# Performance work log

Measured on AMD Instinct MI355X. Metric: run time of the kernel, lower is better.

## Reference

```python
import jax, jax.numpy as jnp
import numpy as np
import math

B, TSRC, TTGT, DM, DI, H = 2, 2048, 2048, 1024, 1024, 16
DH = DI // H
LN_EPS = 1e-5


def setup_inputs() -> dict:
    key = jax.random.key(0)
    ks = iter(jax.random.split(key, 40))
    def p(*shape):
        return jax.random.normal(next(ks), shape, jnp.float32) * 0.02
    inp = {
        "enc_out_vecs": jax.random.normal(next(ks), (B, TSRC, DM), jnp.float32),
        "output_vecs": jax.random.normal(next(ks), (B, TTGT, DM), jnp.float32),
    }
    for tag in ("dd", "ed"):
        inp["Wq_" + tag] = p(DM, DI); inp["bq_" + tag] = jnp.zeros((DI,), jnp.float32)
        inp["Wk_" + tag] = p(DM, DI); inp["bk_" + tag] = jnp.zeros((DI,), jnp.float32)
        inp["Wv_" + tag] = p(DM, DI); inp["bv_" + tag] = jnp.zeros((DI,), jnp.float32)
        inp["Wo_" + tag] = p(DI, DM); inp["bo_" + tag] = jnp.zeros((DM,), jnp.float32)
        inp["W1_" + tag] = p(DM, 2 * DM); inp["b1_" + tag] = jnp.zeros((2 * DM,), jnp.float32)
        inp["W2_" + tag] = p(2 * DM, DM); inp["b2_" + tag] = jnp.zeros((DM,), jnp.float32)
        inp["g1_" + tag] = jnp.ones((DM,), jnp.float32); inp["be1_" + tag] = jnp.zeros((DM,), jnp.float32)
        inp["g2_" + tag] = jnp.ones((DM,), jnp.float32); inp["be2_" + tag] = jnp.zeros((DM,), jnp.float32)
    return inp


def _ln(x, g, b):
    m = jnp.mean(x, axis=-1, keepdims=True)
    v = jnp.var(x, axis=-1, keepdims=True)
    return (x - m) * jax.lax.rsqrt(v + LN_EPS) * g + b


def _mha(xq, xkv, Wq, bq, Wk, bk, Wv, bv, causal):
    Bb, Tq, _ = xq.shape
    Tk = xkv.shape[1]
    q = (xq @ Wq + bq).reshape(Bb, Tq, H, DH)
    k = (xkv @ Wk + bk).reshape(Bb, Tk, H, DH)
    v = (xkv @ Wv + bv).reshape(Bb, Tk, H, DH)
    s = jnp.einsum("bqhd,bkhd->bhqk", q, k) / math.sqrt(DH)
    if causal:
        mask = jnp.where(jnp.arange(Tk)[None, :] > jnp.arange(Tq)[:, None], -jnp.inf, 0.0)
        s = s + mask
    w = jax.nn.softmax(s, axis=-1)
    return jnp.einsum("bhqk,bkhd->bqhd", w, v).reshape(Bb, Tq, H * DH)


def reference(enc_out_vecs, output_vecs,
              Wq_dd, bq_dd, Wk_dd, bk_dd, Wv_dd, bv_dd, Wo_dd, bo_dd,
              W1_dd, b1_dd, W2_dd, b2_dd, g1_dd, be1_dd, g2_dd, be2_dd,
              Wq_ed, bq_ed, Wk_ed, bk_ed, Wv_ed, bv_ed, Wo_ed, bo_ed,
              W1_ed, b1_ed, W2_ed, b2_ed, g1_ed, be1_ed, g2_ed, be2_ed):
    # masked self-attention over decoder inputs
    x = output_vecs
    a = _mha(x, x, Wq_dd, bq_dd, Wk_dd, bk_dd, Wv_dd, bv_dd, causal=True)
    x = _ln(a @ Wo_dd + bo_dd + x, g1_dd, be1_dd)
    x = _ln(x + jax.nn.relu(x @ W1_dd + b1_dd) @ W2_dd + b2_dd, g2_dd, be2_dd)
    # cross attention against encoder outputs
    a = _mha(x, enc_out_vecs, Wq_ed, bq_ed, Wk_ed, bk_ed, Wv_ed, bv_ed, causal=False)
    x = _ln(a @ Wo_ed + bo_ed + x, g1_ed, be1_ed)
    x = _ln(jax.nn.relu(x @ W1_ed + b1_ed) @ W2_ed + b2_ed + x, g2_ed, be2_ed)
    return x
```

## Files before the change

### kernel.cpp

```cpp
#include <hip/hip_runtime.h>
#include <stdint.h>

#define DEV __device__ __forceinline__
typedef unsigned short u16;
typedef __attribute__((ext_vector_type(8))) short bf16x8;
typedef __attribute__((ext_vector_type(4))) float f32x4;

#define AS1 __attribute__((address_space(1)))
#define AS3 __attribute__((address_space(3)))
#define WAITVM0 asm volatile("s_waitcnt vmcnt(0)" ::: "memory")
#define QSCALE 0.18033688011112042f

DEV u16 f2bf(float f) {
  union { float f; uint32_t u; } x; x.f = f;
  uint32_t r = x.u + 0x7fffu + ((x.u >> 16) & 1u);
  return (u16)(r >> 16);
}

DEV uint32_t cvt_pk_bf16(float a, float b) {
  uint32_t r;
  asm("v_cvt_pk_bf16_f32 %0, %1, %2" : "=v"(r) : "v"(a), "v"(b));
  return r;
}

__global__ __launch_bounds__(256) void k_cvt2(const float* __restrict__ a, const float* __restrict__ bsrc,
                                              u16* __restrict__ oa, u16* __restrict__ ob, int n4) {
  int i = blockIdx.x * blockDim.x + threadIdx.x;
  const float* s;
  u16* o;
  int k;
  if (i < n4) { s = a; o = oa; k = i; }
  else        { s = bsrc; o = ob; k = i - n4; }
  float4 v = reinterpret_cast<const float4*>(s)[k];
  reinterpret_cast<ushort4*>(o)[k] = make_ushort4(f2bf(v.x), f2bf(v.y), f2bf(v.z), f2bf(v.w));
}

struct WTJob { const float* W; u16* WT; int K, M, msh, start; };
struct WTJobs { WTJob j[12]; };

__global__ void k_wT_all(WTJobs jobs) {
  __shared__ float tile[32][33];
  int b = blockIdx.x;
  int i = 0;
#pragma unroll
  for (int t = 1; t < 12; ++t)
    if (b >= jobs.j[t].start) i = t;
  const WTJob J = jobs.j[i];
  int rel = b - J.start;
  int m0 = (rel & ((1 << J.msh) - 1)) << 5;
  int k0 = (rel >> J.msh) << 5;
  int tx = threadIdx.x, ty = threadIdx.y;
#pragma unroll
  for (int q = 0; q < 4; ++q)
    tile[ty + q * 8][tx] = J.W[(size_t)(k0 + ty + q * 8) * J.M + m0 + tx];
  __syncthreads();
#pragma unroll
  for (int q = 0; q < 4; ++q)
    J.WT[(size_t)(m0 + ty + q * 8) * J.K + k0 + tx] = f2bf(tile[tx][ty + q * 8]);
}

template<int R>
DEV void stage_tile(const u16* __restrict__ g, int strideElems, u16* lds, int tid, int wv) {
#pragma unroll
  for (int t = 0; t < R / 32; ++t) {
    int idx = t * 256 + tid;
    int row = idx >> 3;
    int b = (idx & 7) << 4;
    int sb = b ^ ((row & 7) << 4);
    const char* src = (const char*)g + (size_t)row * strideElems * 2 + sb;
    char* dst = (char*)lds + (size_t)(t * 256 + wv * 64) * 16;
    __builtin_amdgcn_global_load_lds((const AS1 void*)src, (AS3 void*)dst, 16, 0, 0);
  }
}

DEV bf16x8 lds_frag(const u16* lds, int row, int kel) {
  int off = row * 128 + ((kel * 2) ^ ((row & 7) << 4));
  return *(const bf16x8*)((const char*)lds + off);
}

template<int MODE>
__global__ __launch_bounds__(256) void k_gemm(const u16* __restrict__ A, int lda,
                                              const u16* __restrict__ BT,
                                              const float* __restrict__ bias,
                                              void* __restrict__ C, int ldc, int K) {
  __shared__ __align__(16) u16 A_lds[2][128 * 64];
  __shared__ __align__(16) u16 B_lds[2][128 * 64];
  const int tid = threadIdx.x, lane = tid & 63, wv = tid >> 6;
  const int wm = wv >> 1, wn = wv & 1;
  const int bm0 = blockIdx.y * 128, bn0 = blockIdx.x * 128;
  const int lr = lane & 15, lk = (lane >> 4) * 8, r0 = (lane >> 4) * 4;

  f32x4 acc[4][4];
#pragma unroll
  for (int i = 0; i < 4; ++i)
#pragma unroll
    for (int j = 0; j < 4; ++j) acc[i][j] = f32x4{0.f, 0.f, 0.f, 0.f};

  stage_tile<128>(A + (size_t)bm0 * lda, lda, A_lds[0], tid, wv);
  stage_tile<128>(BT + (size_t)bn0 * K, K, B_lds[0], tid, wv);
  WAITVM0;
  __builtin_amdgcn_s_barrier();

  int cur = 0;
  for (int k0 = 0; k0 < K; k0 += 64) {
    if (k0 + 64 < K) {
      stage_tile<128>(A + (size_t)bm0 * lda + k0 + 64, lda, A_lds[cur ^ 1], tid, wv);
      stage_tile<128>(BT + (size_t)bn0 * K + k0 + 64, K, B_lds[cur ^ 1], tid, wv);
    }
#pragma unroll
    for (int kk = 0; kk < 2; ++kk) {
      bf16x8 af[4], bfr[4];
#pragma unroll
      for (int i = 0; i < 4; ++i) af[i] = lds_frag(A_lds[cur], wm * 64 + i * 16 + lr, kk * 32 + lk);
#pragma unroll
      for (int j = 0; j < 4; ++j) bfr[j] = lds_frag(B_lds[cur], wn * 64 + j * 16 + lr, kk * 32 + lk);
#pragma unroll
      for (int i = 0; i < 4; ++i)
#pragma unroll
        for (int j = 0; j < 4; ++j)
          acc[i][j] = __builtin_amdgcn_mfma_f32_16x16x32_bf16(af[i], bfr[j], acc[i][j], 0, 0, 0);
    }
    WAITVM0;
    __builtin_amdgcn_s_barrier();
    cur ^= 1;
  }

#pragma unroll
  for (int j = 0; j < 4; ++j) {
    int col = bn0 + wn * 64 + j * 16 + lr;
    float bv = bias[col];
#pragma unroll
    for (int i = 0; i < 4; ++i) {
      int rowb = bm0 + wm * 64 + i * 16 + r0;
      if constexpr (MODE == 0) {
#pragma unroll
        for (int r = 0; r < 4; ++r)
          ((float*)C)[(size_t)(rowb + r) * ldc + col] = acc[i][j][r] + bv;
      } else {
#pragma unroll
        for (int r = 0; r < 4; ++r) {
          float v = fmaxf(acc[i][j][r] + bv, 0.f);
          ((u16*)C)[(size_t)(rowb + r) * ldc + col] = f2bf(v);
        }
      }
    }
  }
}

__global__ __launch_bounds__(256) void k_qkv(const u16* __restrict__ Aq, const u16* __restrict__ Akv,
                                             const u16* __restrict__ BT,
                                             const float* __restrict__ bq, const float* __restrict__ bk,
                                             const float* __restrict__ bv,
                                             u16* __restrict__ Qb, u16* __restrict__ Kb,
                                             u16* __restrict__ Vt, int K) {
  __shared__ __align__(16) u16 A_lds[2][128 * 64];
  __shared__ __align__(16) u16 B_lds[2][128 * 64];
  const int tid = threadIdx.x, lane = tid & 63, wv = tid >> 6;
  const int wm = wv >> 1, wn = wv & 1;
  const int bm0 = blockIdx.y * 128, bn0 = blockIdx.x * 128;
  const int seg = bn0 >> 10;
  const u16* A = (seg == 0) ? Aq : Akv;
  const int lr = lane & 15, lk = (lane >> 4) * 8, r0 = (lane >> 4) * 4;

  f32x4 acc[4][4];
#pragma unroll
  for (int i = 0; i < 4; ++i)
#pragma unroll
    for (int j = 0; j < 4; ++j) acc[i][j] = f32x4{0.f, 0.f, 0.f, 0.f};

  stage_tile<128>(A + (size_t)bm0 * K, K, A_lds[0], tid, wv);
  stage_tile<128>(BT + (size_t)bn0 * K, K, B_lds[0], tid, wv);
  WAITVM0;
  __builtin_amdgcn_s_barrier();

  int cur = 0;
  for (int k0 = 0; k0 < K; k0 += 64) {
    if (k0 + 64 < K) {
      stage_tile<128>(A + (size_t)bm0 * K + k0 + 64, K, A_lds[cur ^ 1], tid, wv);
      stage_tile<128>(BT + (size_t)bn0 * K + k0 + 64, K, B_lds[cur ^ 1], tid, wv);
    }
#pragma unroll
    for (int kk = 0; kk < 2; ++kk) {
      bf16x8 af[4], bfr[4];
#pragma unroll
      for (int i = 0; i < 4; ++i) af[i] = lds_frag(A_lds[cur], wm * 64 + i * 16 + lr, kk * 32 + lk);
#pragma unroll
      for (int j = 0; j < 4; ++j) bfr[j] = lds_frag(B_lds[cur], wn * 64 + j * 16 + lr, kk * 32 + lk);
#pragma unroll
      for (int i = 0; i < 4; ++i)
#pragma unroll
        for (int j = 0; j < 4; ++j)
          acc[i][j] = __builtin_amdgcn_mfma_f32_16x16x32_bf16(af[i], bfr[j], acc[i][j], 0, 0, 0);
    }
    WAITVM0;
    __builtin_amdgcn_s_barrier();
    cur ^= 1;
  }

#pragma unroll
  for (int j = 0; j < 4; ++j) {
    int col = bn0 + wn * 64 + j * 16 + lr;
    int cl = col & 1023;
#pragma unroll
    for (int i = 0; i < 4; ++i) {
      int rowb = bm0 + wm * 64 + i * 16 + r0;
      if (seg == 0) {
        float bb = bq[cl];
#pragma unroll
        for (int r = 0; r < 4; ++r)
          Qb[(size_t)(rowb + r) * 1024 + cl] = f2bf((acc[i][j][r] + bb) * QSCALE);
      } else if (seg == 1) {
        float bb = bk[cl];
#pragma unroll
        for (int r = 0; r < 4; ++r)
          Kb[(size_t)(rowb + r) * 1024 + cl] = f2bf(acc[i][j][r] + bb);
      } else {
        float bb = bv[cl];
        int bidx = rowb >> 11, t = rowb & 2047;
        ushort4 o = make_ushort4(f2bf(acc[i][j][0] + bb), f2bf(acc[i][j][1] + bb),
                                 f2bf(acc[i][j][2] + bb), f2bf(acc[i][j][3] + bb));
        *reinterpret_cast<ushort4*>(&Vt[((size_t)bidx * 1024 + cl) * 2048 + t]) = o;
      }
    }
  }
}

__global__ __launch_bounds__(256) void k_ln(const float* __restrict__ Rm, const float* __restrict__ X,
                                            const float* __restrict__ g, const float* __restrict__ be,
                                            float* __restrict__ Y, u16* __restrict__ Yb) {
  int row = blockIdx.x;
  size_t base4 = (size_t)row * 256;
  int t = threadIdx.x;
  float4 a = reinterpret_cast<const float4*>(Rm)[base4 + t];
  float4 x = reinterpret_cast<const float4*>(X)[base4 + t];
  float v0 = a.x + x.x, v1 = a.y + x.y, v2 = a.z + x.z, v3 = a.w + x.w;
  float s = v0 + v1 + v2 + v3;
  float ss = v0 * v0 + v1 * v1 + v2 * v2 + v3 * v3;
#pragma unroll
  for (int m = 1; m < 64; m <<= 1) { s += __shfl_xor(s, m); ss += __shfl_xor(ss, m); }
  __shared__ float red[8];
  int wv = t >> 6;
  if ((t & 63) == 0) { red[wv] = s; red[4 + wv] = ss; }
  __syncthreads();
  s = red[0] + red[1] + red[2] + red[3];
  ss = red[4] + red[5] + red[6] + red[7];
  float mean = s * (1.f / 1024.f);
  float var = ss * (1.f / 1024.f) - mean * mean;
  float rstd = rsqrtf(var + 1e-5f);
  float4 gv = reinterpret_cast<const float4*>(g)[t];
  float4 bv = reinterpret_cast<const float4*>(be)[t];
  float o0 = (v0 - mean) * rstd * gv.x + bv.x;
  float o1 = (v1 - mean) * rstd * gv.y + bv.y;
  float o2 = (v2 - mean) * rstd * gv.z + bv.z;
  float o3 = (v3 - mean) * rstd * gv.w + bv.w;
  reinterpret_cast<float4*>(Y)[base4 + t] = make_float4(o0, o1, o2, o3);
  if (Yb) {
    ushort4 ob = make_ushort4(f2bf(o0), f2bf(o1), f2bf(o2), f2bf(o3));
    reinterpret_cast<ushort4*>(Yb)[base4 + t] = ob;
  }
}

template<bool CAUSAL>
__global__ __launch_bounds__(256) void k_attn(const u16* __restrict__ Q, const u16* __restrict__ Kg,
                                              const u16* __restrict__ Vt, u16* __restrict__ O, int T) {
  __shared__ __align__(16) u16 K_lds[2][64 * 64];
  __shared__ __align__(16) u16 V_lds[2][64 * 64];
  __shared__ __align__(16) u16 p_lds[4][16 * 64];
  const int tid = threadIdx.x, lane = tid & 63, wv = tid >> 6;
  const int h = blockIdx.y, b = blockIdx.z;
  const int qx = CAUSAL ? (gridDim.x - 1 - blockIdx.x) : blockIdx.x;
  const int q0 = qx * 64;
  const int qw = q0 + wv * 16;
  const int lq = lane & 15, g = lane >> 4;
  const int swz = (lq & 7) << 4;
  const int fb0 = lq * 128 + ((g * 16) ^ swz);
  const int fb1 = lq * 128 + ((g * 16 + 64) ^ swz);
  const size_t qkbase = ((size_t)b * T) * 1024 + h * 64;
  const size_t vbase = ((size_t)b * 1024 + h * 64) * T;

  bf16x8 aq0, aq1;
  {
    const u16* qp = Q + qkbase + (size_t)(qw + lq) * 1024 + g * 8;
    aq0 = *reinterpret_cast<const bf16x8*>(qp);
    aq1 = *reinterpret_cast<const bf16x8*>(qp + 32);
  }

  const int srow = tid >> 3;
  const int ssb = ((tid & 7) << 4) ^ ((srow & 7) << 4);
  const char* ksrc = (const char*)(Kg + qkbase) + (size_t)srow * 2048 + ssb;
  const char* vsrc = (const char*)(Vt + vbase) + (size_t)srow * ((size_t)T * 2) + ssb;
  const int vstep2 = T * 64;
  const uint32_t doff = (uint32_t)((tid & 192) << 4);

  auto stage = [&](const char* kp, const char* vp, int buf) {
    char* kd = (char*)K_lds[buf] + doff;
    char* vd = (char*)V_lds[buf] + doff;
    __builtin_amdgcn_global_load_lds((const AS1 void*)kp, (AS3 void*)kd, 16, 0, 0);
    __builtin_amdgcn_global_load_lds((const AS1 void*)(kp + 65536), (AS3 void*)(kd + 4096), 16, 0, 0);
    __builtin_amdgcn_global_load_lds((const AS1 void*)vp, (AS3 void*)vd, 16, 0, 0);
    __builtin_amdgcn_global_load_lds((const AS1 void*)(vp + vstep2), (AS3 void*)(vd + 4096), 16, 0, 0);
  };

  f32x4 acc[4];
#pragma unroll
  for (int j = 0; j < 4; ++j) acc[j] = f32x4{0.f, 0.f, 0.f, 0.f};
  float lsum = 0.f;

  const int nt = CAUSAL ? (qx + 1) : (T >> 6);

  stage(ksrc, vsrc, 0);
  WAITVM0;
  __builtin_amdgcn_s_barrier();
  ksrc += 131072;
  vsrc += 128;

  char* pw = (char*)p_lds[wv];
  int cur = 0;
  for (int it = 0; it < nt; ++it) {
    const int kv0 = it << 6;
    if (it + 1 < nt) {
      stage(ksrc, vsrc, cur ^ 1);
      ksrc += 131072;
      vsrc += 128;
    }
    const char* kb = (const char*)K_lds[cur];
    const char* vb = (const char*)V_lds[cur];
    f32x4 st[4];
    __builtin_amdgcn_s_setprio(1);
#pragma unroll
    for (int j = 0; j < 4; ++j) {
      bf16x8 bk0 = *reinterpret_cast<const bf16x8*>(kb + fb0 + j * 2048);
      bf16x8 bk1 = *reinterpret_cast<const bf16x8*>(kb + fb1 + j * 2048);
      f32x4 t0 = f32x4{0.f, 0.f, 0.f, 0.f};
      t0 = __builtin_amdgcn_mfma_f32_16x16x32_bf16(bk0, aq0, t0, 0, 0, 0);
      t0 = __builtin_amdgcn_mfma_f32_16x16x32_bf16(bk1, aq1, t0, 0, 0, 0);
      st[j] = t0;
    }
    __builtin_amdgcn_s_setprio(0);
    uint32_t pk[8];
    if (CAUSAL && it == nt - 1) {
      const int qrow = qw + lq;
#pragma unroll
      for (int j = 0; j < 4; ++j) {
        float p0 = __builtin_exp2f(st[j][0]);
        float p1 = __builtin_exp2f(st[j][1]);
        float p2 = __builtin_exp2f(st[j][2]);
        float p3 = __builtin_exp2f(st[j][3]);
        int kvb = kv0 + j * 16 + g * 4;
        p0 = (kvb > qrow) ? 0.f : p0;
        p1 = (kvb + 1 > qrow) ? 0.f : p1;
        p2 = (kvb + 2 > qrow) ? 0.f : p2;
        p3 = (kvb + 3 > qrow) ? 0.f : p3;
        lsum += (p0 + p1) + (p2 + p3);
        pk[2 * j] = cvt_pk_bf16(p0, p1);
        pk[2 * j + 1] = cvt_pk_bf16(p2, p3);
      }
    } else {
#pragma unroll
      for (int j = 0; j < 4; ++j) {
        float p0 = __builtin_exp2f(st[j][0]);
        float p1 = __builtin_exp2f(st[j][1]);
        float p2 = __builtin_exp2f(st[j][2]);
        float p3 = __builtin_exp2f(st[j][3]);
        lsum += (p0 + p1) + (p2 + p3);
        pk[2 * j] = cvt_pk_bf16(p0, p1);
        pk[2 * j + 1] = cvt_pk_bf16(p2, p3);
      }
    }
#pragma unroll
    for (int j = 0; j < 4; ++j)
      *reinterpret_cast<uint2*>(pw + lq * 128 + ((j * 32 + g * 8) ^ swz)) =
          make_uint2(pk[2 * j], pk[2 * j + 1]);
    bf16x8 pf0 = *reinterpret_cast<const bf16x8*>(pw + fb0);
    bf16x8 pf1 = *reinterpret_cast<const bf16x8*>(pw + fb1);
    __builtin_amdgcn_s_setprio(1);
#pragma unroll
    for (int j2 = 0; j2 < 4; ++j2) {
      bf16x8 v0 = *reinterpret_cast<const bf16x8*>(vb + fb0 + j2 * 2048);
      bf16x8 v1 = *reinterpret_cast<const bf16x8*>(vb + fb1 + j2 * 2048);
      acc[j2] = __builtin_amdgcn_mfma_f32_16x16x32_bf16(v0, pf0, acc[j2], 0, 0, 0);
      acc[j2] = __builtin_amdgcn_mfma_f32_16x16x32_bf16(v1, pf1, acc[j2], 0, 0, 0);
    }
    __builtin_amdgcn_s_setprio(0);
    WAITVM0;
    __builtin_amdgcn_s_barrier();
    cur ^= 1;
  }

  lsum += __shfl_xor(lsum, 16);
  lsum += __shfl_xor(lsum, 32);
  float inv = 1.f / lsum;
  size_t rb = qkbase + (size_t)(qw + lq) * 1024;
#pragma unroll
  for (int j2 = 0; j2 < 4; ++j2) {
    ushort4 o = make_ushort4(f2bf(acc[j2][0] * inv), f2bf(acc[j2][1] * inv),
                             f2bf(acc[j2][2] * inv), f2bf(acc[j2][3] * inv));
    *reinterpret_cast<ushort4*>(&O[rb + j2 * 16 + g * 4]) = o;
  }
}

extern "C" void kernel_launch(void* const* d_in, const int* in_sizes, int n_in,
                              void* d_out, int out_size, void* d_ws, size_t ws_size,
                              hipStream_t stream) {
  const int T = 2048;
  const float* enc = (const float*)d_in[0];
  const float* outv = (const float*)d_in[1];
  auto F = [&](int i) { return (const float*)d_in[i]; };

  size_t off = 0;
  auto alloc = [&](size_t bytes) {
    void* p = (char*)d_ws + off;
    off += (bytes + 255) & ~(size_t)255;
    return p;
  };

  const int tdK[12] = {1024, 1024, 1024, 1024, 1024, 2048, 1024, 1024, 1024, 1024, 1024, 2048};
  const int tdM[12] = {1024, 1024, 1024, 1024, 2048, 1024, 1024, 1024, 1024, 1024, 2048, 1024};
  const int tdIdx[12] = {2, 4, 6, 8, 10, 12, 18, 20, 22, 24, 26, 28};
  u16* WT_[12];
  for (int i = 0; i < 12; ++i) WT_[i] = (u16*)alloc((size_t)tdK[i] * tdM[i] * 2);

  u16* Xb0 = (u16*)alloc(4096ull * 1024 * 2);
  u16* Eb = (u16*)alloc(4096ull * 1024 * 2);
  u16* Qb = (u16*)alloc(4096ull * 1024 * 2);
  u16* Kb = (u16*)alloc(4096ull * 1024 * 2);
  u16* Vt = (u16*)alloc(4096ull * 1024 * 2);
  u16* Ab = (u16*)alloc(4096ull * 1024 * 2);
  u16* Hb = (u16*)alloc(4096ull * 2048 * 2);
  u16* Xbc = (u16*)alloc(4096ull * 1024 * 2);
  float* Rf = (float*)alloc(4096ull * 1024 * 4);
  float* Xfa = (float*)alloc(4096ull * 1024 * 4);
  float* Xfb = (float*)alloc(4096ull * 1024 * 4);

  k_cvt2<<<8192, 256, 0, stream>>>(outv, enc, Xb0, Eb, 4096 * 1024 / 4);

  WTJobs jobs;
  int start = 0;
  for (int i = 0; i < 12; ++i) {
    int msh = (tdM[i] == 2048) ? 6 : 5;
    jobs.j[i] = {F(tdIdx[i]), WT_[i], tdK[i], tdM[i], msh, start};
    start += (tdM[i] >> 5) * (tdK[i] >> 5);
  }
  k_wT_all<<<start, dim3(32, 8), 0, stream>>>(jobs);

  dim3 gq(24, 32);
  dim3 g1k(8, 32);
  dim3 g2k(16, 32);
  dim3 ga(32, 16, 2);

  k_qkv<<<gq, 256, 0, stream>>>(Xb0, Xb0, WT_[0], F(3), F(5), F(7), Qb, Kb, Vt, 1024);
  k_attn<true><<<ga, 256, 0, stream>>>(Qb, Kb, Vt, Ab, T);
  k_gemm<0><<<g1k, 256, 0, stream>>>(Ab, 1024, WT_[3], F(9), Rf, 1024, 1024);
  k_ln<<<4096, 256, 0, stream>>>(Rf, outv, F(14), F(15), Xfa, Xbc);
  k_gemm<2><<<g2k, 256, 0, stream>>>(Xbc, 1024, WT_[4], F(11), Hb, 2048, 1024);
  k_gemm<0><<<g1k, 256, 0, stream>>>(Hb, 2048, WT_[5], F(13), Rf, 1024, 2048);
  k_ln<<<4096, 256, 0, stream>>>(Rf, Xfa, F(16), F(17), Xfb, Xbc);

  k_qkv<<<gq, 256, 0, stream>>>(Xbc, Eb, WT_[6], F(19), F(21), F(23), Qb, Kb, Vt, 1024);
  k_attn<false><<<ga, 256, 0, stream>>>(Qb, Kb, Vt, Ab, T);
  k_gemm<0><<<g1k, 256, 0, stream>>>(Ab, 1024, WT_[9], F(25), Rf, 1024, 1024);
  k_ln<<<4096, 256, 0, stream>>>(Rf, Xfb, F(30), F(31), Xfa, Xbc);
  k_gemm<2><<<g2k, 256, 0, stream>>>(Xbc, 1024, WT_[10], F(27), Hb, 2048, 1024);
  k_gemm<0><<<g1k, 256, 0, stream>>>(Hb, 2048, WT_[11], F(29), Rf, 1024, 2048);
  k_ln<<<4096, 256, 0, stream>>>(Rf, Xfa, F(32), F(33), (float*)d_out, (u16*)nullptr);
}
```

Measured before the change: 486.1 us.

## Shrink GEMM N-tile, triple-buffer loads, swizzle blocks, pair causal attention q-tiles

GEMM and QKV kernels now use 128x64 tiles with a three-stage global-to-LDS pipeline and partial vmcnt waits, which doubles the grid and remaps block indices into an XCD-aware order. The aim is better occupancy and overlap of memory loads with compute across the 256 CUs. Causal attention launches half as many blocks, and each block processes a long query tile together with its mirror short tile while sharing the staged K/V. This balances work across blocks but adds register pressure and smaller MFMA reuse per tile.

```diff
diff --git a/kernel.cpp b/kernel.cpp
--- a/kernel.cpp
+++ b/kernel.cpp
@@ -83,51 +83,61 @@
                                               const u16* __restrict__ BT,
                                               const float* __restrict__ bias,
                                               void* __restrict__ C, int ldc, int K) {
-  __shared__ __align__(16) u16 A_lds[2][128 * 64];
-  __shared__ __align__(16) u16 B_lds[2][128 * 64];
+  __shared__ __align__(16) u16 A_lds[3][128 * 64];
+  __shared__ __align__(16) u16 B_lds[3][64 * 64];
   const int tid = threadIdx.x, lane = tid & 63, wv = tid >> 6;
   const int wm = wv >> 1, wn = wv & 1;
-  const int bm0 = blockIdx.y * 128, bn0 = blockIdx.x * 128;
+  const int nwg = gridDim.x * gridDim.y;
+  const int flat = blockIdx.y * gridDim.x + blockIdx.x;
+  const int sw = (flat & 7) * (nwg >> 3) + (flat >> 3);
+  const int bx = sw % gridDim.x, by = sw / gridDim.x;
+  const int bm0 = by * 128, bn0 = bx * 64;
   const int lr = lane & 15, lk = (lane >> 4) * 8, r0 = (lane >> 4) * 4;
 
-  f32x4 acc[4][4];
+  f32x4 acc[4][2];
 #pragma unroll
   for (int i = 0; i < 4; ++i)
 #pragma unroll
-    for (int j = 0; j < 4; ++j) acc[i][j] = f32x4{0.f, 0.f, 0.f, 0.f};
-
-  stage_tile<128>(A + (size_t)bm0 * lda, lda, A_lds[0], tid, wv);
-  stage_tile<128>(BT + (size_t)bn0 * K, K, B_lds[0], tid, wv);
-  WAITVM0;
-  __builtin_amdgcn_s_barrier();
-
-  int cur = 0;
-  for (int k0 = 0; k0 < K; k0 += 64) {
-    if (k0 + 64 < K) {
-      stage_tile<128>(A + (size_t)bm0 * lda + k0 + 64, lda, A_lds[cur ^ 1], tid, wv);
-      stage_tile<128>(BT + (size_t)bn0 * K + k0 + 64, K, B_lds[cur ^ 1], tid, wv);
-    }
+    for (int j = 0; j < 2; ++j) acc[i][j] = f32x4{0.f, 0.f, 0.f, 0.f};
+
+  auto stageT = [&](int s, int t) {
+    stage_tile<128>(A + (size_t)bm0 * lda + t * 64, lda, A_lds[s], tid, wv);
+    stage_tile<64>(BT + (size_t)bn0 * K + t * 64, K, B_lds[s], tid, wv);
+  };
+
+  const int nt = K >> 6;
+  stageT(0, 0);
+  stageT(1, 1);
+  for (int t = 0; t < nt; ++t) {
+    if (t + 2 < nt) {
+      stageT((t + 2) % 3, t + 2);
+      asm volatile("s_waitcnt vmcnt(12)" ::: "memory");
+    } else if (t + 1 < nt) {
+      asm volatile("s_waitcnt vmcnt(6)" ::: "memory");
+    } else {
+      asm volatile("s_waitcnt vmcnt(0)" ::: "memory");
+    }
+    __builtin_amdgcn_s_barrier();
+    const int cur = t % 3;
 #pragma unroll
     for (int kk = 0; kk < 2; ++kk) {
-      bf16x8 af[4], bfr[4];
+      bf16x8 af[4], bfr[2];
 #pragma unroll
       for (int i = 0; i < 4; ++i) af[i] = lds_frag(A_lds[cur], wm * 64 + i * 16 + lr, kk * 32 + lk);
 #pragma unroll
-      for (int j = 0; j < 4; ++j) bfr[j] = lds_frag(B_lds[cur], wn * 64 + j * 16 + lr, kk * 32 + lk);
+      for (int j = 0; j < 2; ++j) bfr[j] = lds_frag(B_lds[cur], wn * 32 + j * 16 + lr, kk * 32 + lk);
 #pragma unroll
       for (int i = 0; i < 4; ++i)
 #pragma unroll
-        for (int j = 0; j < 4; ++j)
+        for (int j = 0; j < 2; ++j)
           acc[i][j] = __builtin_amdgcn_mfma_f32_16x16x32_bf16(af[i], bfr[j], acc[i][j], 0, 0, 0);
     }
-    WAITVM0;
     __builtin_amdgcn_s_barrier();
-    cur ^= 1;
-  }
-
-#pragma unroll
-  for (int j = 0; j < 4; ++j) {
-    int col = bn0 + wn * 64 + j * 16 + lr;
+  }
+
+#pragma unroll
+  for (int j = 0; j < 2; ++j) {
+    int col = bn0 + wn * 32 + j * 16 + lr;
     float bv = bias[col];
 #pragma unroll
     for (int i = 0; i < 4; ++i) {
@@ -153,53 +163,63 @@
                                              const float* __restrict__ bv,
                                              u16* __restrict__ Qb, u16* __restrict__ Kb,
                                              u16* __restrict__ Vt, int K) {
-  __shared__ __align__(16) u16 A_lds[2][128 * 64];
-  __shared__ __align__(16) u16 B_lds[2][128 * 64];
+  __shared__ __align__(16) u16 A_lds[3][128 * 64];
+  __shared__ __align__(16) u16 B_lds[3][64 * 64];
   const int tid = threadIdx.x, lane = tid & 63, wv = tid >> 6;
   const int wm = wv >> 1, wn = wv & 1;
-  const int bm0 = blockIdx.y * 128, bn0 = blockIdx.x * 128;
+  const int nwg = gridDim.x * gridDim.y;
+  const int flat = blockIdx.y * gridDim.x + blockIdx.x;
+  const int sw = (flat & 7) * (nwg >> 3) + (flat >> 3);
+  const int bx = sw % gridDim.x, by = sw / gridDim.x;
+  const int bm0 = by * 128, bn0 = bx * 64;
   const int seg = bn0 >> 10;
   const u16* A = (seg == 0) ? Aq : Akv;
   const int lr = lane & 15, lk = (lane >> 4) * 8, r0 = (lane >> 4) * 4;
 
-  f32x4 acc[4][4];
+  f32x4 acc[4][2];
 #pragma unroll
   for (int i = 0; i < 4; ++i)
 #pragma unroll
-    for (int j = 0; j < 4; ++j) acc[i][j] = f32x4{0.f, 0.f, 0.f, 0.f};
-
-  stage_tile<128>(A + (size_t)bm0 * K, K, A_lds[0], tid, wv);
-  stage_tile<128>(BT + (size_t)bn0 * K, K, B_lds[0], tid, wv);
-  WAITVM0;
-  __builtin_amdgcn_s_barrier();
-
-  int cur = 0;
-  for (int k0 = 0; k0 < K; k0 += 64) {
-    if (k0 + 64 < K) {
-      stage_tile<128>(A + (size_t)bm0 * K + k0 + 64, K, A_lds[cur ^ 1], tid, wv);
-      stage_tile<128>(BT + (size_t)bn0 * K + k0 + 64, K, B_lds[cur ^ 1], tid, wv);
-    }
+    for (int j = 0; j < 2; ++j) acc[i][j] = f32x4{0.f, 0.f, 0.f, 0.f};
+
+  auto stageT = [&](int s, int t) {
+    stage_tile<128>(A + (size_t)bm0 * K + t * 64, K, A_lds[s], tid, wv);
+    stage_tile<64>(BT + (size_t)bn0 * K + t * 64, K, B_lds[s], tid, wv);
+  };
+
+  const int nt = K >> 6;
+  stageT(0, 0);
+  stageT(1, 1);
+  for (int t = 0; t < nt; ++t) {
+    if (t + 2 < nt) {
+      stageT((t + 2) % 3, t + 2);
+      asm volatile("s_waitcnt vmcnt(12)" ::: "memory");
+    } else if (t + 1 < nt) {
+      asm volatile("s_waitcnt vmcnt(6)" ::: "memory");
+    } else {
+      asm volatile("s_waitcnt vmcnt(0)" ::: "memory");
+    }
+    __builtin_amdgcn_s_barrier();
+    const int cur = t % 3;
 #pragma unroll
     for (int kk = 0; kk < 2; ++kk) {
-      bf16x8 af[4], bfr[4];
+      bf16x8 af[4], bfr[2];
 #pragma unroll
       for (int i = 0; i < 4; ++i) af[i] = lds_frag(A_lds[cur], wm * 64 + i * 16 + lr, kk * 32 + lk);
 #pragma unroll
-      for (int j = 0; j < 4; ++j) bfr[j] = lds_frag(B_lds[cur], wn * 64 + j * 16 + lr, kk * 32 + lk);
+      for (int j = 0; j < 2; ++j) bfr[j] = lds_frag(B_lds[cur], wn * 32 + j * 16 + lr, kk * 32 + lk);
 #pragma unroll
       for (int i = 0; i < 4; ++i)
 #pragma unroll
-        for (int j = 0; j < 4; ++j)
+        for (int j = 0; j < 2; ++j)
           acc[i][j] = __builtin_amdgcn_mfma_f32_16x16x32_bf16(af[i], bfr[j], acc[i][j], 0, 0, 0);
     }
-    WAITVM0;
     __builtin_amdgcn_s_barrier();
-    cur ^= 1;
-  }
-
-#pragma unroll
-  for (int j = 0; j < 4; ++j) {
-    int col = bn0 + wn * 64 + j * 16 + lr;
+  }
+
+#pragma unroll
+  for (int j = 0; j < 2; ++j) {
+    int col = bn0 + wn * 32 + j * 16 + lr;
     int cl = col & 1023;
 #pragma unroll
     for (int i = 0; i < 4; ++i) {
@@ -268,9 +288,6 @@
   __shared__ __align__(16) u16 p_lds[4][16 * 64];
   const int tid = threadIdx.x, lane = tid & 63, wv = tid >> 6;
   const int h = blockIdx.y, b = blockIdx.z;
-  const int qx = CAUSAL ? (gridDim.x - 1 - blockIdx.x) : blockIdx.x;
-  const int q0 = qx * 64;
-  const int qw = q0 + wv * 16;
   const int lq = lane & 15, g = lane >> 4;
   const int swz = (lq & 7) << 4;
   const int fb0 = lq * 128 + ((g * 16) ^ swz);
@@ -278,11 +295,21 @@
   const size_t qkbase = ((size_t)b * T) * 1024 + h * 64;
   const size_t vbase = ((size_t)b * 1024 + h * 64) * T;
 
-  bf16x8 aq0, aq1;
+  const int qp = CAUSAL ? (31 - blockIdx.x) : blockIdx.x;
+  const int qa = CAUSAL ? blockIdx.x : 0;
+  const int nt = CAUSAL ? (qp + 1) : (T >> 6);
+  const int qwP = qp * 64 + wv * 16, qwA = qa * 64 + wv * 16;
+
+  bf16x8 aqP0, aqP1, aqA0, aqA1;
   {
-    const u16* qp = Q + qkbase + (size_t)(qw + lq) * 1024 + g * 8;
-    aq0 = *reinterpret_cast<const bf16x8*>(qp);
-    aq1 = *reinterpret_cast<const bf16x8*>(qp + 32);
+    const u16* qp_ = Q + qkbase + (size_t)(qwP + lq) * 1024 + g * 8;
+    aqP0 = *reinterpret_cast<const bf16x8*>(qp_);
+    aqP1 = *reinterpret_cast<const bf16x8*>(qp_ + 32);
+    if constexpr (CAUSAL) {
+      const u16* qa_ = Q + qkbase + (size_t)(qwA + lq) * 1024 + g * 8;
+      aqA0 = *reinterpret_cast<const bf16x8*>(qa_);
+      aqA1 = *reinterpret_cast<const bf16x8*>(qa_ + 32);
+    }
   }
 
   const int srow = tid >> 3;
@@ -301,30 +328,15 @@
     __builtin_amdgcn_global_load_lds((const AS1 void*)(vp + vstep2), (AS3 void*)(vd + 4096), 16, 0, 0);
   };
 
-  f32x4 acc[4];
-#pragma unroll
-  for (int j = 0; j < 4; ++j) acc[j] = f32x4{0.f, 0.f, 0.f, 0.f};
-  float lsum = 0.f;
-
-  const int nt = CAUSAL ? (qx + 1) : (T >> 6);
-
-  stage(ksrc, vsrc, 0);
-  WAITVM0;
-  __builtin_amdgcn_s_barrier();
-  ksrc += 131072;
-  vsrc += 128;
+  f32x4 accP[4], accA[4];
+  float lsumP = 0.f, lsumA = 0.f;
+#pragma unroll
+  for (int j = 0; j < 4; ++j) { accP[j] = f32x4{0.f, 0.f, 0.f, 0.f}; accA[j] = f32x4{0.f, 0.f, 0.f, 0.f}; }
 
   char* pw = (char*)p_lds[wv];
-  int cur = 0;
-  for (int it = 0; it < nt; ++it) {
-    const int kv0 = it << 6;
-    if (it + 1 < nt) {
-      stage(ksrc, vsrc, cur ^ 1);
-      ksrc += 131072;
-      vsrc += 128;
-    }
-    const char* kb = (const char*)K_lds[cur];
-    const char* vb = (const char*)V_lds[cur];
+
+  auto qstep = [&](bf16x8 a0, bf16x8 a1, int qrow, bool domask, int kv0,
+                   f32x4* acc, float& lsum, const char* kb, const char* vb) {
     f32x4 st[4];
     __builtin_amdgcn_s_setprio(1);
 #pragma unroll
@@ -332,14 +344,13 @@
       bf16x8 bk0 = *reinterpret_cast<const bf16x8*>(kb + fb0 + j * 2048);
       bf16x8 bk1 = *reinterpret_cast<const bf16x8*>(kb + fb1 + j * 2048);
       f32x4 t0 = f32x4{0.f, 0.f, 0.f, 0.f};
-      t0 = __builtin_amdgcn_mfma_f32_16x16x32_bf16(bk0, aq0, t0, 0, 0, 0);
-      t0 = __builtin_amdgcn_mfma_f32_16x16x32_bf16(bk1, aq1, t0, 0, 0, 0);
+      t0 = __builtin_amdgcn_mfma_f32_16x16x32_bf16(bk0, a0, t0, 0, 0, 0);
+      t0 = __builtin_amdgcn_mfma_f32_16x16x32_bf16(bk1, a1, t0, 0, 0, 0);
       st[j] = t0;
     }
     __builtin_amdgcn_s_setprio(0);
     uint32_t pk[8];
-    if (CAUSAL && it == nt - 1) {
-      const int qrow = qw + lq;
+    if (domask) {
 #pragma unroll
       for (int j = 0; j < 4; ++j) {
         float p0 = __builtin_exp2f(st[j][0]);
@@ -382,20 +393,55 @@
       acc[j2] = __builtin_amdgcn_mfma_f32_16x16x32_bf16(v1, pf1, acc[j2], 0, 0, 0);
     }
     __builtin_amdgcn_s_setprio(0);
+  };
+
+  stage(ksrc, vsrc, 0);
+  WAITVM0;
+  __builtin_amdgcn_s_barrier();
+  ksrc += 131072;
+  vsrc += 128;
+
+  int cur = 0;
+  for (int it = 0; it < nt; ++it) {
+    const int kv0 = it << 6;
+    if (it + 1 < nt) {
+      stage(ksrc, vsrc, cur ^ 1);
+      ksrc += 131072;
+      vsrc += 128;
+    }
+    const char* kb = (const char*)K_lds[cur];
+    const char* vb = (const char*)V_lds[cur];
+    qstep(aqP0, aqP1, qwP + lq, CAUSAL && it == qp, kv0, accP, lsumP, kb, vb);
+    if constexpr (CAUSAL) {
+      if (it <= qa)
+        qstep(aqA0, aqA1, qwA + lq, it == qa, kv0, accA, lsumA, kb, vb);
+    }
     WAITVM0;
     __builtin_amdgcn_s_barrier();
     cur ^= 1;
   }
 
-  lsum += __shfl_xor(lsum, 16);
-  lsum += __shfl_xor(lsum, 32);
-  float inv = 1.f / lsum;
-  size_t rb = qkbase + (size_t)(qw + lq) * 1024;
+  lsumP += __shfl_xor(lsumP, 16);
+  lsumP += __shfl_xor(lsumP, 32);
+  float invP = 1.f / lsumP;
+  size_t rbP = qkbase + (size_t)(qwP + lq) * 1024;
 #pragma unroll
   for (int j2 = 0; j2 < 4; ++j2) {
-    ushort4 o = make_ushort4(f2bf(acc[j2][0] * inv), f2bf(acc[j2][1] * inv),
-                             f2bf(acc[j2][2] * inv), f2bf(acc[j2][3] * inv));
-    *reinterpret_cast<ushort4*>(&O[rb + j2 * 16 + g * 4]) = o;
+    ushort4 o = make_ushort4(f2bf(accP[j2][0] * invP), f2bf(accP[j2][1] * invP),
+                             f2bf(accP[j2][2] * invP), f2bf(accP[j2][3] * invP));
+    *reinterpret_cast<ushort4*>(&O[rbP + j2 * 16 + g * 4]) = o;
+  }
+  if constexpr (CAUSAL) {
+    lsumA += __shfl_xor(lsumA, 16);
+    lsumA += __shfl_xor(lsumA, 32);
+    float invA = 1.f / lsumA;
+    size_t rbA = qkbase + (size_t)(qwA + lq) * 1024;
+#pragma unroll
+    for (int j2 = 0; j2 < 4; ++j2) {
+      ushort4 o = make_ushort4(f2bf(accA[j2][0] * invA), f2bf(accA[j2][1] * invA),
+                               f2bf(accA[j2][2] * invA), f2bf(accA[j2][3] * invA));
+      *reinterpret_cast<ushort4*>(&O[rbA + j2 * 16 + g * 4]) = o;
+    }
   }
 }
 
@@ -443,13 +489,14 @@
   }
   k_wT_all<<<start, dim3(32, 8), 0, stream>>>(jobs);
 
-  dim3 gq(24, 32);
-  dim3 g1k(8, 32);
-  dim3 g2k(16, 32);
-  dim3 ga(32, 16, 2);
+  dim3 gq(48, 32);
+  dim3 g1k(16, 32);
+  dim3 g2k(32, 32);
+  dim3 gac(16, 16, 2);
+  dim3 gan(32, 16, 2);
 
   k_qkv<<<gq, 256, 0, stream>>>(Xb0, Xb0, WT_[0], F(3), F(5), F(7), Qb, Kb, Vt, 1024);
-  k_attn<true><<<ga, 256, 0, stream>>>(Qb, Kb, Vt, Ab, T);
+  k_attn<true><<<gac, 256, 0, stream>>>(Qb, Kb, Vt, Ab, T);
   k_gemm<0><<<g1k, 256, 0, stream>>>(Ab, 1024, WT_[3], F(9), Rf, 1024, 1024);
   k_ln<<<4096, 256, 0, stream>>>(Rf, outv, F(14), F(15), Xfa, Xbc);
   k_gemm<2><<<g2k, 256, 0, stream>>>(Xbc, 1024, WT_[4], F(11), Hb, 2048, 1024);
@@ -457,7 +504,7 @@
   k_ln<<<4096, 256, 0, stream>>>(Rf, Xfa, F(16), F(17), Xfb, Xbc);
 
   k_qkv<<<gq, 256, 0, stream>>>(Xbc, Eb, WT_[6], F(19), F(21), F(23), Qb, Kb, Vt, 1024);
-  k_attn<false><<<ga, 256, 0, stream>>>(Qb, Kb, Vt, Ab, T);
+  k_attn<false><<<gan, 256, 0, stream>>>(Qb, Kb, Vt, Ab, T);
   k_gemm<0><<<g1k, 256, 0, stream>>>(Ab, 1024, WT_[9], F(25), Rf, 1024, 1024);
   k_ln<<<4096, 256, 0, stream>>>(Rf, Xfb, F(30), F(31), Xfa, Xbc);
   k_gemm<2><<<g2k, 256, 0, stream>>>(Xbc, 1024, WT_[10], F(27), Hb, 2048, 1024);
```

New measurement: 442.0 us. -9.1%, faster.
